# Performance work log

Measured on AMD Instinct MI355X. Metric: run time of the kernel, lower is better.

Reference implementation:

```python
import jax, jax.numpy as jnp
import numpy as np

VOCAB = 50000
WORD_DIM = 300
PAT_LEN = 6
DOC_LEN = 32768


def setup_inputs() -> dict:
    key = jax.random.key(0)
    k1, k2, k3, k4 = jax.random.split(key, 4)
    doc = jax.random.randint(k1, (DOC_LEN,), 0, VOCAB, dtype=jnp.int64)
    embeddings = jax.random.normal(k2, (VOCAB, WORD_DIM), dtype=jnp.float32)
    w = jax.random.normal(k3, (PAT_LEN, PAT_LEN, WORD_DIM), dtype=jnp.float32)
    # original code normalizes each w[i, j] to unit norm at init
    w = w / jnp.linalg.norm(w, axis=-1, keepdims=True)
    b = jax.random.normal(k4, (PAT_LEN, PAT_LEN), dtype=jnp.float32)
    return {"doc": doc, "embeddings": embeddings, "w": w, "b": b}


def reference(doc, embeddings, w, b):
    p = w.shape[0]
    # Only the superdiagonal (i, i+1) of the transition matrix is nonzero.
    idx = jnp.arange(p - 1)
    w_sd = w[idx, idx + 1]          # [p-1, d]
    b_sd = b[idx, idx + 1]          # [p-1]

    x = embeddings[doc]             # [T, d] embedding gather
    # vals[t, i] = sigmoid(w[i,i+1] . x_t + b[i,i+1])   -> [T, p-1]
    vals = jax.nn.sigmoid(x @ w_sd.T + b_sd)

    start = jnp.zeros((p,), dtype=vals.dtype).at[0].set(1.0)

    def step(hidden, v_t):
        # hidden @ T_t: new[j] = hidden[j-1] * vals[t, j-1] for j >= 1
        shifted = hidden[:-1] * v_t                       # [p-1]
        new_hidden = jnp.concatenate([jnp.zeros((1,), hidden.dtype), shifted]) + start
        return new_hidden, new_hidden[-1]                 # score contribution = hidden @ final

    _, contribs = jax.lax.scan(step, start, vals)
    return jnp.sum(contribs)
```

## Files before the change

kernel.cpp:

```cpp
#include <hip/hip_runtime.h>

#define T_LEN 32768
#define DIM   300
#define NP    5
#define TB    16
#define HALO  4

__device__ __forceinline__ float fast_sigmoid(float z) {
    return 1.0f / (1.0f + __expf(-z));
}

__global__ __launch_bounds__(256) void softpat_kernel(
    const int*   __restrict__ doc,
    const float* __restrict__ emb,
    const float* __restrict__ w,
    const float* __restrict__ b,
    float*       __restrict__ out)
{
    __shared__ float lds_w[NP][DIM];
    __shared__ float lds_b[NP];
    __shared__ float lds_v[TB + HALO][NP];

    const int tid  = threadIdx.x;
    const int lane = tid & 63;
    const int wave = tid >> 6;
    const int t0   = blockIdx.x * TB;

    for (int idx = tid; idx < NP * DIM; idx += 256) {
        int i = idx / DIM;
        int d = idx - i * DIM;
        lds_w[i][d] = w[(7 * i + 1) * DIM + d];
    }
    if (tid < NP) lds_b[tid] = b[7 * tid + 1];
    __syncthreads();

    for (int k = 0; k < 5; ++k) {
        const int tt = (k < 4) ? (wave * 4 + k) : (TB + wave);
        const int t  = t0 + tt;
        const bool valid = (t < T_LEN);

        float a0 = 0.f, a1 = 0.f, a2 = 0.f, a3 = 0.f, a4 = 0.f;
        if (valid) {
            const float* __restrict__ xrow = emb + (size_t)doc[t] * DIM;
            #pragma unroll
            for (int it = 0; it < 5; ++it) {
                const int d = it * 64 + lane;
                if (d < DIM) {
                    const float x = xrow[d];
                    a0 += x * lds_w[0][d];
                    a1 += x * lds_w[1][d];
                    a2 += x * lds_w[2][d];
                    a3 += x * lds_w[3][d];
                    a4 += x * lds_w[4][d];
                }
            }
        }
        #pragma unroll
        for (int off = 32; off > 0; off >>= 1) {
            a0 += __shfl_xor(a0, off);
            a1 += __shfl_xor(a1, off);
            a2 += __shfl_xor(a2, off);
            a3 += __shfl_xor(a3, off);
            a4 += __shfl_xor(a4, off);
        }
        if (lane == 0) {
            lds_v[tt][0] = valid ? fast_sigmoid(a0 + lds_b[0]) : 0.f;
            lds_v[tt][1] = valid ? fast_sigmoid(a1 + lds_b[1]) : 0.f;
            lds_v[tt][2] = valid ? fast_sigmoid(a2 + lds_b[2]) : 0.f;
            lds_v[tt][3] = valid ? fast_sigmoid(a3 + lds_b[3]) : 0.f;
            lds_v[tt][4] = valid ? fast_sigmoid(a4 + lds_b[4]) : 0.f;
        }
    }
    __syncthreads();

    if (wave == 0) {
        float p = 0.f;
        const int s = t0 + lane;
        if (lane < TB && s <= T_LEN - (NP)) {
            p = lds_v[lane + 0][0] * lds_v[lane + 1][1] * lds_v[lane + 2][2]
              * lds_v[lane + 3][3] * lds_v[lane + 4][4];
        }
        #pragma unroll
        for (int off = 32; off > 0; off >>= 1) p += __shfl_xor(p, off);
        if (lane == 0) atomicAdd(out, p);
    }
}

extern "C" void kernel_launch(void* const* d_in, const int* in_sizes, int n_in,
                              void* d_out, int out_size, void* d_ws, size_t ws_size,
                              hipStream_t stream) {
    const int*   doc = (const int*)  d_in[0];
    const float* emb = (const float*)d_in[1];
    const float* w   = (const float*)d_in[2];
    const float* b   = (const float*)d_in[3];
    float*       out = (float*)d_out;

    hipMemsetAsync(out, 0, sizeof(float), stream);

    const int blocks = T_LEN / TB;
    softpat_kernel<<<blocks, 256, 0, stream>>>(doc, emb, w, b, out);
}
```

Measured before the change: 124.9 us.

## Split into vals and reduce kernels with float4 loads and 16-lane token groups

Splits the fused kernel into two. The first kernel computes the sigmoid values for each token using 16-lane groups and float4 loads of both the embedding rows and the LDS weights. It writes them to a workspace buffer. This removes the redundant halo recomputation (20 rows computed per 16 tokens) and the full 64-lane shuffle reductions. The second kernel forms the diagonal products and reduces them with one atomic per block, at the cost of an extra launch and a round trip through global memory for the values.

Result: faster. 102.6 us (-17.8%).

```diff
diff --git a/kernel.cpp b/kernel.cpp
--- a/kernel.cpp
+++ b/kernel.cpp
@@ -2,88 +2,96 @@
 
 #define T_LEN 32768
 #define DIM   300
+#define NCH   75
 #define NP    5
-#define TB    16
-#define HALO  4
 
 __device__ __forceinline__ float fast_sigmoid(float z) {
     return 1.0f / (1.0f + __expf(-z));
 }
 
-__global__ __launch_bounds__(256) void softpat_kernel(
+__global__ __launch_bounds__(256) void vals_kernel(
     const int*   __restrict__ doc,
     const float* __restrict__ emb,
     const float* __restrict__ w,
     const float* __restrict__ b,
-    float*       __restrict__ out)
+    float*       __restrict__ vals)
 {
     __shared__ float lds_w[NP][DIM];
     __shared__ float lds_b[NP];
-    __shared__ float lds_v[TB + HALO][NP];
 
-    const int tid  = threadIdx.x;
-    const int lane = tid & 63;
-    const int wave = tid >> 6;
-    const int t0   = blockIdx.x * TB;
+    const int tid = threadIdx.x;
 
-    for (int idx = tid; idx < NP * DIM; idx += 256) {
-        int i = idx / DIM;
-        int d = idx - i * DIM;
-        lds_w[i][d] = w[(7 * i + 1) * DIM + d];
+    for (int c = tid; c < NP * NCH; c += 256) {
+        const int i  = c / NCH;
+        const int cc = c - i * NCH;
+        const float4 v = *reinterpret_cast<const float4*>(w + (size_t)(7 * i + 1) * DIM + 4 * cc);
+        *reinterpret_cast<float4*>(&lds_w[i][4 * cc]) = v;
     }
     if (tid < NP) lds_b[tid] = b[7 * tid + 1];
     __syncthreads();
 
-    for (int k = 0; k < 5; ++k) {
-        const int tt = (k < 4) ? (wave * 4 + k) : (TB + wave);
-        const int t  = t0 + tt;
-        const bool valid = (t < T_LEN);
+    const int g   = tid >> 4;
+    const int sub = tid & 15;
+    const int t   = blockIdx.x * 16 + g;
 
-        float a0 = 0.f, a1 = 0.f, a2 = 0.f, a3 = 0.f, a4 = 0.f;
-        if (valid) {
-            const float* __restrict__ xrow = emb + (size_t)doc[t] * DIM;
-            #pragma unroll
-            for (int it = 0; it < 5; ++it) {
-                const int d = it * 64 + lane;
-                if (d < DIM) {
-                    const float x = xrow[d];
-                    a0 += x * lds_w[0][d];
-                    a1 += x * lds_w[1][d];
-                    a2 += x * lds_w[2][d];
-                    a3 += x * lds_w[3][d];
-                    a4 += x * lds_w[4][d];
-                }
-            }
-        }
-        #pragma unroll
-        for (int off = 32; off > 0; off >>= 1) {
-            a0 += __shfl_xor(a0, off);
-            a1 += __shfl_xor(a1, off);
-            a2 += __shfl_xor(a2, off);
-            a3 += __shfl_xor(a3, off);
-            a4 += __shfl_xor(a4, off);
-        }
-        if (lane == 0) {
-            lds_v[tt][0] = valid ? fast_sigmoid(a0 + lds_b[0]) : 0.f;
-            lds_v[tt][1] = valid ? fast_sigmoid(a1 + lds_b[1]) : 0.f;
-            lds_v[tt][2] = valid ? fast_sigmoid(a2 + lds_b[2]) : 0.f;
-            lds_v[tt][3] = valid ? fast_sigmoid(a3 + lds_b[3]) : 0.f;
-            lds_v[tt][4] = valid ? fast_sigmoid(a4 + lds_b[4]) : 0.f;
+    const float* __restrict__ xrow = emb + (size_t)doc[t] * DIM;
+
+    float a0 = 0.f, a1 = 0.f, a2 = 0.f, a3 = 0.f, a4 = 0.f;
+    #pragma unroll
+    for (int r = 0; r < 5; ++r) {
+        const int c = sub + 16 * r;
+        if (c < NCH) {
+            const float4 xv = *reinterpret_cast<const float4*>(xrow + 4 * c);
+            const float4 w0 = *reinterpret_cast<const float4*>(&lds_w[0][4 * c]);
+            const float4 w1 = *reinterpret_cast<const float4*>(&lds_w[1][4 * c]);
+            const float4 w2 = *reinterpret_cast<const float4*>(&lds_w[2][4 * c]);
+            const float4 w3 = *reinterpret_cast<const float4*>(&lds_w[3][4 * c]);
+            const float4 w4 = *reinterpret_cast<const float4*>(&lds_w[4][4 * c]);
+            a0 += xv.x * w0.x + xv.y * w0.y + xv.z * w0.z + xv.w * w0.w;
+            a1 += xv.x * w1.x + xv.y * w1.y + xv.z * w1.z + xv.w * w1.w;
+            a2 += xv.x * w2.x + xv.y * w2.y + xv.z * w2.z + xv.w * w2.w;
+            a3 += xv.x * w3.x + xv.y * w3.y + xv.z * w3.z + xv.w * w3.w;
+            a4 += xv.x * w4.x + xv.y * w4.y + xv.z * w4.z + xv.w * w4.w;
         }
     }
+
+    #pragma unroll
+    for (int off = 8; off >= 1; off >>= 1) {
+        a0 += __shfl_xor(a0, off);
+        a1 += __shfl_xor(a1, off);
+        a2 += __shfl_xor(a2, off);
+        a3 += __shfl_xor(a3, off);
+        a4 += __shfl_xor(a4, off);
+    }
+
+    if (sub < NP) {
+        const float a = (sub == 0) ? a0 : (sub == 1) ? a1 : (sub == 2) ? a2
+                       : (sub == 3) ? a3 : a4;
+        vals[sub * T_LEN + t] = fast_sigmoid(a + lds_b[sub]);
+    }
+}
+
+__global__ __launch_bounds__(256) void reduce_kernel(
+    const float* __restrict__ vals,
+    float*       __restrict__ out)
+{
+    const int s = blockIdx.x * 256 + threadIdx.x;
+    float p = 0.f;
+    if (s <= T_LEN - NP) {
+        p = vals[s]
+          * vals[1 * T_LEN + s + 1]
+          * vals[2 * T_LEN + s + 2]
+          * vals[3 * T_LEN + s + 3]
+          * vals[4 * T_LEN + s + 4];
+    }
+    #pragma unroll
+    for (int off = 32; off >= 1; off >>= 1) p += __shfl_xor(p, off);
+
+    __shared__ float partial[4];
+    if ((threadIdx.x & 63) == 0) partial[threadIdx.x >> 6] = p;
     __syncthreads();
-
-    if (wave == 0) {
-        float p = 0.f;
-        const int s = t0 + lane;
-        if (lane < TB && s <= T_LEN - (NP)) {
-            p = lds_v[lane + 0][0] * lds_v[lane + 1][1] * lds_v[lane + 2][2]
-              * lds_v[lane + 3][3] * lds_v[lane + 4][4];
-        }
-        #pragma unroll
-        for (int off = 32; off > 0; off >>= 1) p += __shfl_xor(p, off);
-        if (lane == 0) atomicAdd(out, p);
-    }
+    if (threadIdx.x == 0)
+        atomicAdd(out, partial[0] + partial[1] + partial[2] + partial[3]);
 }
 
 extern "C" void kernel_launch(void* const* d_in, const int* in_sizes, int n_in,
@@ -94,9 +102,10 @@
     const float* w   = (const float*)d_in[2];
     const float* b   = (const float*)d_in[3];
     float*       out = (float*)d_out;
+    float*       vals = (float*)d_ws;
 
     hipMemsetAsync(out, 0, sizeof(float), stream);
 
-    const int blocks = T_LEN / TB;
-    softpat_kernel<<<blocks, 256, 0, stream>>>(doc, emb, w, b, out);
+    vals_kernel<<<T_LEN / 16, 256, 0, stream>>>(doc, emb, w, b, vals);
+    reduce_kernel<<<(T_LEN + 255) / 256, 256, 0, stream>>>(vals, out);
 }
```
